# Optimization experiments

Hardware: AMD Instinct MI355X
Metric: run time of the kernel (lower is better)

The kernel has to match this reference:

```python
import jax, jax.numpy as jnp
import numpy as np

B, C, H, W = 2, 128, 48, 48
N = H * W
NQ = 25               # number of quantization bins (r2d2 default)
K_RELIABILITY = 0.5   # self.k
A = (NQ - 1) / 2.0    # quantizer slope over score range [-1, 1]
RADIUS = 4            # label window: [x-4 : x+5, y-4 : y+5]

# ---- quantizer line coefficients (r2d2 quantized AP) ----
# first half: q1 = -a*s + (a*min + [nq..1]);  special bin 0 -> constant 1
# second half: q2 =  a*s + ([2-nq..1] - a*min); special last bin -> constant 1
_W1 = jnp.full((NQ,), -A, jnp.float32).at[0].set(0.0)
_B1 = (jnp.arange(NQ, 0, -1, dtype=jnp.float32) - A).at[0].set(1.0)
_W2 = jnp.full((NQ,), A, jnp.float32).at[-1].set(0.0)
_B2 = (jnp.arange(2 - NQ, 2, dtype=jnp.float32) + A).at[-1].set(1.0)

# ---- ground-truth label matrix (static): pixel j positive for query i iff within 9x9 window ----
_row = np.arange(N) // W
_col = np.arange(N) % W
_L = ((np.abs(_row[:, None] - _row[None, :]) <= RADIUS) &
      (np.abs(_col[:, None] - _col[None, :]) <= RADIUS)).astype(np.float32)
LABEL = jnp.asarray(_L)  # (N, N)


def grid_sample_bilinear(img, grid):
    """torch.F.grid_sample: bilinear, zero padding, align_corners=False.
    img: (C, H, W); grid: (Hg, Wg, 2) in [-1, 1] -> out (C, Hg, Wg)."""
    Ci, Hi, Wi = img.shape
    ix = ((grid[..., 0] + 1.0) * Wi - 1.0) * 0.5
    iy = ((grid[..., 1] + 1.0) * Hi - 1.0) * 0.5
    x0 = jnp.floor(ix); y0 = jnp.floor(iy)
    wx1 = ix - x0; wy1 = iy - y0

    def gather(xi, yi):
        valid = (xi >= 0) & (xi < Wi) & (yi >= 0) & (yi < Hi)
        xc = jnp.clip(xi, 0, Wi - 1).astype(jnp.int32)
        yc = jnp.clip(yi, 0, Hi - 1).astype(jnp.int32)
        return img[:, yc, xc] * valid.astype(img.dtype)  # (C, Hg, Wg)

    return (gather(x0, y0) * (1 - wx1) * (1 - wy1)
            + gather(x0 + 1, y0) * wx1 * (1 - wy1)
            + gather(x0, y0 + 1) * (1 - wx1) * wy1
            + gather(x0 + 1, y0 + 1) * wx1 * wy1)


def quantized_ap(S, labels):
    """S: (N, M) similarity scores in [-1,1]; labels: (N, M) in {0,1}. Returns AP (N,)."""
    s = S[:, None, :]                                      # (N, 1, M)
    q1 = _W1[None, :, None] * s + _B1[None, :, None]        # (N, NQ, M)
    q2 = _W2[None, :, None] * s + _B2[None, :, None]
    q = jnp.maximum(jnp.minimum(q1, q2), 0.0)               # triangular bin weights
    nbs = q.sum(-1)                                         # (N, NQ) all counts per bin
    rec = jnp.einsum('ncm,nm->nc', q, labels)               # (N, NQ) positive counts per bin
    prec = jnp.cumsum(rec, -1) / (1e-16 + jnp.cumsum(nbs, -1))
    return (prec * rec).sum(-1) / rec.sum(-1)               # (N,)


def _loss_one(query_desc, db_desc, rel_map, g):
    db = grid_sample_bilinear(db_desc, g)                   # (C, H, W)
    Q = query_desc.reshape(C, N).T                          # (N, C)
    D = db.reshape(C, N).T                                  # (M=N, C)
    S = Q @ D.T                                             # (N, M) cosine scores
    ap = quantized_ap(S, LABEL)                             # (N,)
    r = rel_map.reshape(-1)                                 # (N,)
    return jnp.mean(1.0 - (ap * r + K_RELIABILITY * (1.0 - r)))


def setup_inputs() -> dict:
    key = jax.random.key(0)
    k1, k2, k3, k4 = jax.random.split(key, 4)
    d1 = jax.random.normal(k1, (B, C, H, W), jnp.float32)
    d1 = d1 / jnp.linalg.norm(d1, axis=1, keepdims=True)
    d2 = jax.random.normal(k2, (B, C, H, W), jnp.float32)
    d2 = d2 / jnp.linalg.norm(d2, axis=1, keepdims=True)
    rel = jax.random.uniform(k3, (B, 1, H, W), jnp.float32)
    grid = jax.random.uniform(k4, (B, H, W, 2), jnp.float32, minval=-1.0, maxval=1.0)
    return {"image1_descriptor": d1, "image2_descriptor": d2,
            "reliability": rel, "grid": grid}


def reference(image1_descriptor, image2_descriptor, reliability, grid):
    per_image = jax.vmap(_loss_one)(image1_descriptor, image2_descriptor,
                                    reliability[:, 0], grid)
    return per_image.mean()
```

## Files before the change

### kernel.cpp

```cpp
#include <hip/hip_runtime.h>
#include <hip/hip_bf16.h>

#define BB 2
#define CC 128
#define HH 48
#define WW 48
#define NN (HH*WW)
#define PB 26
#define HST 27
#define QT 16
#define MT 64
#define MSPLIT 4
#define NTILES (NN/QT)
#define ITERS (NN/MSPLIT/MT)
#define SLICE (QT*PB)
#define PSCALE 65536.0f
#define PINV   (1.0f/65536.0f)

typedef __bf16 bf16x8 __attribute__((ext_vector_type(8)));
typedef float  f32x4  __attribute__((ext_vector_type(4)));
typedef unsigned short u16;
typedef unsigned int   u32;

static __device__ __forceinline__ u16 f2bf(float x) {
    __hip_bfloat16 h = __float2bfloat16(x);
    return __builtin_bit_cast(u16, h);
}

__global__ __launch_bounds__(256)
void k_prep(const float* __restrict__ img1, const float* __restrict__ img2,
            const float* __restrict__ grid, u16* __restrict__ Qt,
            u16* __restrict__ Dt, float* __restrict__ out) {
    int blk = blockIdx.x;
    if (blk == 0 && threadIdx.x == 0) out[0] = 0.0f;
    bool isg = blk >= 144;
    int bb  = isg ? blk - 144 : blk;
    int bm  = (bb >> 3) * 256 + threadIdx.x;
    int cc0 = (bb & 7) * 16;
    int b   = bm / NN;
    int p   = bm - b * NN;
    u16 tmp[16];
    if (!isg) {
        const float* im = img1 + (size_t)b * CC * NN + (size_t)cc0 * NN;
        #pragma unroll
        for (int c = 0; c < 16; ++c) tmp[c] = f2bf(im[(size_t)c * NN + p]);
        uint4* dst = reinterpret_cast<uint4*>(Qt + (size_t)bm * CC + cc0);
        dst[0] = *reinterpret_cast<uint4*>(&tmp[0]);
        dst[1] = *reinterpret_cast<uint4*>(&tmp[8]);
    } else {
        float gx = grid[bm * 2 + 0];
        float gy = grid[bm * 2 + 1];
        float ix = ((gx + 1.0f) * (float)WW - 1.0f) * 0.5f;
        float iy = ((gy + 1.0f) * (float)HH - 1.0f) * 0.5f;
        float x0f = floorf(ix), y0f = floorf(iy);
        float wx1 = ix - x0f, wy1 = iy - y0f;
        float wx0 = 1.0f - wx1, wy0 = 1.0f - wy1;
        int x0 = (int)x0f, y0 = (int)y0f;
        bool xv0 = (x0 >= 0) && (x0 < WW);
        bool xv1 = (x0 + 1 >= 0) && (x0 + 1 < WW);
        bool yv0 = (y0 >= 0) && (y0 < HH);
        bool yv1 = (y0 + 1 >= 0) && (y0 + 1 < HH);
        int x0c = min(max(x0, 0), WW - 1), x1c = min(max(x0 + 1, 0), WW - 1);
        int y0c = min(max(y0, 0), HH - 1), y1c = min(max(y0 + 1, 0), HH - 1);
        float w00 = (xv0 && yv0) ? wx0 * wy0 : 0.0f;
        float w01 = (xv1 && yv0) ? wx1 * wy0 : 0.0f;
        float w10 = (xv0 && yv1) ? wx0 * wy1 : 0.0f;
        float w11 = (xv1 && yv1) ? wx1 * wy1 : 0.0f;
        int p00 = y0c * WW + x0c, p01 = y0c * WW + x1c;
        int p10 = y1c * WW + x0c, p11 = y1c * WW + x1c;
        const float* im = img2 + (size_t)b * CC * NN + (size_t)cc0 * NN;
        #pragma unroll
        for (int c = 0; c < 16; ++c) {
            const float* pl = im + (size_t)c * NN;
            tmp[c] = f2bf(pl[p00] * w00 + pl[p01] * w01 + pl[p10] * w10 + pl[p11] * w11);
        }
        uint4* dst = reinterpret_cast<uint4*>(Dt + (size_t)bm * CC + cc0);
        dst[0] = *reinterpret_cast<uint4*>(&tmp[0]);
        dst[1] = *reinterpret_cast<uint4*>(&tmp[8]);
    }
}

__global__ __launch_bounds__(256)
void k_main(const u16* __restrict__ Qt, const u16* __restrict__ Dt,
            float* __restrict__ Hall, float* __restrict__ Hpos) {
    __shared__ u16  Qs[QT * 136];
    __shared__ u16  Ds[MT * 136];
    __shared__ float priv[256 * HST];
    __shared__ u32   poshu[QT * PB];

    int tid  = threadIdx.x;
    int bidx = blockIdx.x;
    int b     = bidx / (NTILES * MSPLIT);
    int rem   = bidx % (NTILES * MSPLIT);
    int ntile = rem / MSPLIT;
    int ms    = rem % MSPLIT;
    int n0 = ntile * QT;

    for (int i = tid; i < 256 * HST; i += 256) priv[i] = 0.0f;
    for (int i = tid; i < QT * PB; i += 256) poshu[i] = 0u;
    {
        int row = tid >> 4, col = tid & 15;
        *reinterpret_cast<uint4*>(&Qs[row * 136 + col * 8]) =
            *reinterpret_cast<const uint4*>(Qt + ((size_t)(b * NN + n0 + row)) * CC + col * 8);
    }
    int lane = tid & 63, wave = tid >> 6, quad = lane >> 4, l15 = lane & 15;
    int q  = l15;
    int n  = n0 + q;
    int rn = n / WW, cn = n % WW;
    float* ph = &priv[tid * HST];

    int mstart = ms * (NN / MSPLIT);
    for (int it = 0; it < ITERS; ++it) {
        int m0 = mstart + it * MT;
        __syncthreads();
        #pragma unroll
        for (int k = 0; k < 4; ++k) {
            int idx = tid + k * 256;
            int row = idx >> 4, col = idx & 15;
            *reinterpret_cast<uint4*>(&Ds[row * 136 + col * 8]) =
                *reinterpret_cast<const uint4*>(Dt + ((size_t)(b * NN + m0 + row)) * CC + col * 8);
        }
        __syncthreads();

        f32x4 acc = {0.f, 0.f, 0.f, 0.f};
        #pragma unroll
        for (int kc = 0; kc < 4; ++kc) {
            bf16x8 av = *reinterpret_cast<const bf16x8*>(&Ds[(wave * 16 + l15) * 136 + kc * 32 + quad * 8]);
            bf16x8 bv = *reinterpret_cast<const bf16x8*>(&Qs[l15 * 136 + kc * 32 + quad * 8]);
            acc = __builtin_amdgcn_mfma_f32_16x16x32_bf16(av, bv, acc, 0, 0, 0);
        }

        int mb = m0 + wave * 16 + quad * 4;
        #pragma unroll
        for (int i = 0; i < 4; ++i) {
            float s  = acc[i];
            float t  = fminf(fmaxf(fmaf(-12.0f, s, 12.0f), 0.0f), 24.0f);
            float cf = floorf(t);
            float f  = t - cf;
            int   c0 = (int)cf;
            float h0 = ph[c0], h1 = ph[c0 + 1];
            ph[c0]     = h0 + (1.0f - f);
            ph[c0 + 1] = h1 + f;
            int m  = mb + i;
            int rm = m / WW, cm = m - rm * WW;
            int dr = rn - rm, dc = cn - cm;
            if ((unsigned)(dr + 4) <= 8u && (unsigned)(dc + 4) <= 8u) {
                u32 w0 = (u32)(fmaf(-PSCALE, f, PSCALE) + 0.5f);
                u32 w1 = (u32)(f * PSCALE + 0.5f);
                atomicAdd(&poshu[q * PB + c0],     w0);
                atomicAdd(&poshu[q * PB + c0 + 1], w1);
            }
        }
    }
    __syncthreads();
    float* oa = Hall + (size_t)bidx * SLICE;
    float* op = Hpos + (size_t)bidx * SLICE;
    for (int idx = tid; idx < SLICE; idx += 256) {
        int c = idx >> 4, qq = idx & 15;
        float s2 = 0.0f;
        #pragma unroll
        for (int j = 0; j < 16; ++j) s2 += priv[(j * 16 + qq) * HST + c];
        oa[idx] = s2;
        op[idx] = (float)poshu[qq * PB + c] * PINV;
    }
}

__global__ __launch_bounds__(256)
void k_finalize(const float* __restrict__ Hall, const float* __restrict__ Hpos,
                const float* __restrict__ rel, float* __restrict__ out) {
    int gid = blockIdx.x * 256 + threadIdx.x;
    int b = gid / NN, nloc = gid % NN;
    int ntile = nloc >> 4, qq = nloc & 15;
    size_t base = ((size_t)(b * NTILES + ntile) * MSPLIT) * SLICE + qq;
    const float* ha = Hall + base;
    const float* hp = Hpos + base;
    float cumr = 0.f, cumn = 0.f, apn = 0.f, totr = 0.f;
    #pragma unroll
    for (int c = 0; c < 25; ++c) {
        float a = 0.f, r = 0.f;
        #pragma unroll
        for (int s = 0; s < MSPLIT; ++s) {
            a += ha[(size_t)s * SLICE + c * 16];
            r += hp[(size_t)s * SLICE + c * 16];
        }
        cumr += r; cumn += a;
        apn  += (cumr / (1e-16f + cumn)) * r;
        totr += r;
    }
    float ap = apn / totr;
    float rl = rel[gid];
    float loss = 1.0f - (ap * rl + 0.5f * (1.0f - rl));

    for (int off = 32; off > 0; off >>= 1) loss += __shfl_down(loss, off, 64);
    __shared__ float wsum[4];
    int ln = threadIdx.x & 63, wv = threadIdx.x >> 6;
    if (ln == 0) wsum[wv] = loss;
    __syncthreads();
    if (threadIdx.x == 0) {
        float t = wsum[0] + wsum[1] + wsum[2] + wsum[3];
        atomicAdd(out, t * (1.0f / (float)(BB * NN)));
    }
}

extern "C" void kernel_launch(void* const* d_in, const int* in_sizes, int n_in,
                              void* d_out, int out_size, void* d_ws, size_t ws_size,
                              hipStream_t stream) {
    const float* img1 = (const float*)d_in[0];
    const float* img2 = (const float*)d_in[1];
    const float* rel  = (const float*)d_in[2];
    const float* grid = (const float*)d_in[3];

    char* ws = (char*)d_ws;
    const size_t qt_bytes   = (size_t)BB * NN * CC * sizeof(u16);
    const size_t part_bytes = (size_t)BB * NTILES * MSPLIT * SLICE * sizeof(float);
    u16*   Qt   = (u16*)ws;
    u16*   Dt   = (u16*)(ws + qt_bytes);
    float* Hall = (float*)(ws + 2 * qt_bytes);
    float* Hpos = (float*)(ws + 2 * qt_bytes + part_bytes);

    k_prep    <<<288, 256, 0, stream>>>(img1, img2, grid, Qt, Dt, (float*)d_out);
    k_main    <<<BB * NTILES * MSPLIT, 256, 0, stream>>>(Qt, Dt, Hall, Hpos);
    k_finalize<<<(BB * NN) / 256, 256, 0, stream>>>(Hall, Hpos, rel, (float*)d_out);
}
```

Before: 98.80 us.

## Load MFMA operands directly into registers and fuse finalize via last-block counter

The main kernel no longer stages Q and D tiles through shared memory. Each lane loads its bf16 operand fragments straight from global memory into registers and prefetches the next D tile one iteration ahead. This removes two barriers per iteration and the LDS tile buffers. The separate finalize kernel is replaced by an atomic per-group counter, zeroed in the prep kernel, so the last of the MSPLIT blocks for a query tile combines the partial histograms, computes AP and adds to the output. This saves a kernel launch and a pass over global memory, at the cost of thread fences, an atomic counter per group, and more redundant global loads of D rows, since they are no longer shared through LDS.

```diff
diff --git a/kernel.cpp b/kernel.cpp
--- a/kernel.cpp
+++ b/kernel.cpp
@@ -30,8 +30,9 @@
 __global__ __launch_bounds__(256)
 void k_prep(const float* __restrict__ img1, const float* __restrict__ img2,
             const float* __restrict__ grid, u16* __restrict__ Qt,
-            u16* __restrict__ Dt, float* __restrict__ out) {
+            u16* __restrict__ Dt, u32* __restrict__ cnt, float* __restrict__ out) {
     int blk = blockIdx.x;
+    if (threadIdx.x == 0) cnt[blk] = 0u;
     if (blk == 0 && threadIdx.x == 0) out[0] = 0.0f;
     bool isg = blk >= 144;
     int bb  = isg ? blk - 144 : blk;
@@ -82,11 +83,12 @@
 
 __global__ __launch_bounds__(256)
 void k_main(const u16* __restrict__ Qt, const u16* __restrict__ Dt,
-            float* __restrict__ Hall, float* __restrict__ Hpos) {
-    __shared__ u16  Qs[QT * 136];
-    __shared__ u16  Ds[MT * 136];
+            float* __restrict__ Hall, float* __restrict__ Hpos,
+            u32* __restrict__ cnt, const float* __restrict__ rel,
+            float* __restrict__ out) {
     __shared__ float priv[256 * HST];
     __shared__ u32   poshu[QT * PB];
+    __shared__ int   lastflag;
 
     int tid  = threadIdx.x;
     int bidx = blockIdx.x;
@@ -94,61 +96,67 @@
     int rem   = bidx % (NTILES * MSPLIT);
     int ntile = rem / MSPLIT;
     int ms    = rem % MSPLIT;
-    int n0 = ntile * QT;
+    int n0  = ntile * QT;
+    int grp = b * NTILES + ntile;
 
     for (int i = tid; i < 256 * HST; i += 256) priv[i] = 0.0f;
     for (int i = tid; i < QT * PB; i += 256) poshu[i] = 0u;
-    {
-        int row = tid >> 4, col = tid & 15;
-        *reinterpret_cast<uint4*>(&Qs[row * 136 + col * 8]) =
-            *reinterpret_cast<const uint4*>(Qt + ((size_t)(b * NN + n0 + row)) * CC + col * 8);
-    }
+
     int lane = tid & 63, wave = tid >> 6, quad = lane >> 4, l15 = lane & 15;
     int q  = l15;
     int n  = n0 + q;
     int rn = n / WW, cn = n % WW;
     float* ph = &priv[tid * HST];
 
+    const u16* qrow = Qt + ((size_t)(b * NN + n0 + l15)) * CC + quad * 8;
+    bf16x8 bv0 = *reinterpret_cast<const bf16x8*>(qrow);
+    bf16x8 bv1 = *reinterpret_cast<const bf16x8*>(qrow + 32);
+    bf16x8 bv2 = *reinterpret_cast<const bf16x8*>(qrow + 64);
+    bf16x8 bv3 = *reinterpret_cast<const bf16x8*>(qrow + 96);
+
+    __syncthreads();
+
     int mstart = ms * (NN / MSPLIT);
+    const u16* arow = Dt + ((size_t)(b * NN + mstart + wave * 16 + l15)) * CC + quad * 8;
+    bf16x8 a0 = *reinterpret_cast<const bf16x8*>(arow);
+    bf16x8 a1 = *reinterpret_cast<const bf16x8*>(arow + 32);
+    bf16x8 a2 = *reinterpret_cast<const bf16x8*>(arow + 64);
+    bf16x8 a3 = *reinterpret_cast<const bf16x8*>(arow + 96);
+
     for (int it = 0; it < ITERS; ++it) {
-        int m0 = mstart + it * MT;
-        __syncthreads();
-        #pragma unroll
-        for (int k = 0; k < 4; ++k) {
-            int idx = tid + k * 256;
-            int row = idx >> 4, col = idx & 15;
-            *reinterpret_cast<uint4*>(&Ds[row * 136 + col * 8]) =
-                *reinterpret_cast<const uint4*>(Dt + ((size_t)(b * NN + m0 + row)) * CC + col * 8);
-        }
-        __syncthreads();
-
+        bf16x8 c0 = a0, c1 = a1, c2 = a2, c3 = a3;
+        if (it + 1 < ITERS) {
+            const u16* nx = arow + (size_t)(it + 1) * MT * CC;
+            a0 = *reinterpret_cast<const bf16x8*>(nx);
+            a1 = *reinterpret_cast<const bf16x8*>(nx + 32);
+            a2 = *reinterpret_cast<const bf16x8*>(nx + 64);
+            a3 = *reinterpret_cast<const bf16x8*>(nx + 96);
+        }
         f32x4 acc = {0.f, 0.f, 0.f, 0.f};
-        #pragma unroll
-        for (int kc = 0; kc < 4; ++kc) {
-            bf16x8 av = *reinterpret_cast<const bf16x8*>(&Ds[(wave * 16 + l15) * 136 + kc * 32 + quad * 8]);
-            bf16x8 bv = *reinterpret_cast<const bf16x8*>(&Qs[l15 * 136 + kc * 32 + quad * 8]);
-            acc = __builtin_amdgcn_mfma_f32_16x16x32_bf16(av, bv, acc, 0, 0, 0);
-        }
-
-        int mb = m0 + wave * 16 + quad * 4;
+        acc = __builtin_amdgcn_mfma_f32_16x16x32_bf16(c0, bv0, acc, 0, 0, 0);
+        acc = __builtin_amdgcn_mfma_f32_16x16x32_bf16(c1, bv1, acc, 0, 0, 0);
+        acc = __builtin_amdgcn_mfma_f32_16x16x32_bf16(c2, bv2, acc, 0, 0, 0);
+        acc = __builtin_amdgcn_mfma_f32_16x16x32_bf16(c3, bv3, acc, 0, 0, 0);
+
+        int mb = mstart + it * MT + wave * 16 + quad * 4;
         #pragma unroll
         for (int i = 0; i < 4; ++i) {
             float s  = acc[i];
             float t  = fminf(fmaxf(fmaf(-12.0f, s, 12.0f), 0.0f), 24.0f);
             float cf = floorf(t);
             float f  = t - cf;
-            int   c0 = (int)cf;
-            float h0 = ph[c0], h1 = ph[c0 + 1];
-            ph[c0]     = h0 + (1.0f - f);
-            ph[c0 + 1] = h1 + f;
+            int   c0b = (int)cf;
+            float h0 = ph[c0b], h1 = ph[c0b + 1];
+            ph[c0b]     = h0 + (1.0f - f);
+            ph[c0b + 1] = h1 + f;
             int m  = mb + i;
             int rm = m / WW, cm = m - rm * WW;
             int dr = rn - rm, dc = cn - cm;
             if ((unsigned)(dr + 4) <= 8u && (unsigned)(dc + 4) <= 8u) {
                 u32 w0 = (u32)(fmaf(-PSCALE, f, PSCALE) + 0.5f);
                 u32 w1 = (u32)(f * PSCALE + 0.5f);
-                atomicAdd(&poshu[q * PB + c0],     w0);
-                atomicAdd(&poshu[q * PB + c0 + 1], w1);
+                atomicAdd(&poshu[q * PB + c0b],     w0);
+                atomicAdd(&poshu[q * PB + c0b + 1], w1);
             }
         }
     }
@@ -163,42 +171,46 @@
         oa[idx] = s2;
         op[idx] = (float)poshu[qq * PB + c] * PINV;
     }
-}
-
-__global__ __launch_bounds__(256)
-void k_finalize(const float* __restrict__ Hall, const float* __restrict__ Hpos,
-                const float* __restrict__ rel, float* __restrict__ out) {
-    int gid = blockIdx.x * 256 + threadIdx.x;
-    int b = gid / NN, nloc = gid % NN;
-    int ntile = nloc >> 4, qq = nloc & 15;
-    size_t base = ((size_t)(b * NTILES + ntile) * MSPLIT) * SLICE + qq;
-    const float* ha = Hall + base;
-    const float* hp = Hpos + base;
-    float cumr = 0.f, cumn = 0.f, apn = 0.f, totr = 0.f;
-    #pragma unroll
-    for (int c = 0; c < 25; ++c) {
-        float a = 0.f, r = 0.f;
+    __threadfence();
+    __syncthreads();
+    if (tid == 0) {
+        u32 old = atomicAdd(&cnt[grp], 1u);
+        lastflag = (old == MSPLIT - 1);
+    }
+    __syncthreads();
+    if (!lastflag) return;
+
+    __threadfence();
+    float* comb = priv;
+    const float* ga = Hall + (size_t)grp * MSPLIT * SLICE;
+    const float* gp = Hpos + (size_t)grp * MSPLIT * SLICE;
+    for (int idx = tid; idx < SLICE; idx += 256) {
+        float sa = 0.f, sp = 0.f;
         #pragma unroll
         for (int s = 0; s < MSPLIT; ++s) {
-            a += ha[(size_t)s * SLICE + c * 16];
-            r += hp[(size_t)s * SLICE + c * 16];
-        }
-        cumr += r; cumn += a;
-        apn  += (cumr / (1e-16f + cumn)) * r;
-        totr += r;
-    }
-    float ap = apn / totr;
-    float rl = rel[gid];
-    float loss = 1.0f - (ap * rl + 0.5f * (1.0f - rl));
-
-    for (int off = 32; off > 0; off >>= 1) loss += __shfl_down(loss, off, 64);
-    __shared__ float wsum[4];
-    int ln = threadIdx.x & 63, wv = threadIdx.x >> 6;
-    if (ln == 0) wsum[wv] = loss;
-    __syncthreads();
-    if (threadIdx.x == 0) {
-        float t = wsum[0] + wsum[1] + wsum[2] + wsum[3];
-        atomicAdd(out, t * (1.0f / (float)(BB * NN)));
+            sa += ga[(size_t)s * SLICE + idx];
+            sp += gp[(size_t)s * SLICE + idx];
+        }
+        comb[idx]         = sa;
+        comb[SLICE + idx] = sp;
+    }
+    __syncthreads();
+    if (tid < 16) {
+        float cumr = 0.f, cumn = 0.f, apn = 0.f, totr = 0.f;
+        #pragma unroll
+        for (int c = 0; c < 25; ++c) {
+            float a = comb[c * 16 + tid];
+            float r = comb[SLICE + c * 16 + tid];
+            cumr += r; cumn += a;
+            apn  += (cumr / (1e-16f + cumn)) * r;
+            totr += r;
+        }
+        float ap = apn / totr;
+        float rl = rel[b * NN + n0 + tid];
+        float loss = 1.0f - (ap * rl + 0.5f * (1.0f - rl));
+        #pragma unroll
+        for (int off = 8; off > 0; off >>= 1) loss += __shfl_down(loss, off, 16);
+        if (tid == 0) atomicAdd(out, loss * (1.0f / (float)(BB * NN)));
     }
 }
 
@@ -217,8 +229,8 @@
     u16*   Dt   = (u16*)(ws + qt_bytes);
     float* Hall = (float*)(ws + 2 * qt_bytes);
     float* Hpos = (float*)(ws + 2 * qt_bytes + part_bytes);
-
-    k_prep    <<<288, 256, 0, stream>>>(img1, img2, grid, Qt, Dt, (float*)d_out);
-    k_main    <<<BB * NTILES * MSPLIT, 256, 0, stream>>>(Qt, Dt, Hall, Hpos);
-    k_finalize<<<(BB * NN) / 256, 256, 0, stream>>>(Hall, Hpos, rel, (float*)d_out);
-}
+    u32*   cnt  = (u32*)  (ws + 2 * qt_bytes + 2 * part_bytes);
+
+    k_prep<<<288, 256, 0, stream>>>(img1, img2, grid, Qt, Dt, cnt, (float*)d_out);
+    k_main<<<BB * NTILES * MSPLIT, 256, 0, stream>>>(Qt, Dt, Hall, Hpos, cnt, rel, (float*)d_out);
+}
```

Result: slower. 225.7 us (+128.5%).

## Load MFMA operands directly from global into registers with prefetch, drop LDS staging

Applied to the files above, without the earlier changes.

Removes the shared-memory tiles for Q and D. Each wave now loads its MFMA fragments directly from global memory into registers, keeps the Q fragments resident for the whole loop, and prefetches the next D fragment while the current one is consumed. This drops two __syncthreads per iteration and the LDS round trip, and frees shared memory, which may help occupancy. The cost is per-lane 16-byte global loads with a strided row pattern and extra registers for double-buffered fragments.

```diff
diff --git a/kernel.cpp b/kernel.cpp
--- a/kernel.cpp
+++ b/kernel.cpp
@@ -83,8 +83,6 @@
 __global__ __launch_bounds__(256)
 void k_main(const u16* __restrict__ Qt, const u16* __restrict__ Dt,
             float* __restrict__ Hall, float* __restrict__ Hpos) {
-    __shared__ u16  Qs[QT * 136];
-    __shared__ u16  Ds[MT * 136];
     __shared__ float priv[256 * HST];
     __shared__ u32   poshu[QT * PB];
 
@@ -98,57 +96,62 @@
 
     for (int i = tid; i < 256 * HST; i += 256) priv[i] = 0.0f;
     for (int i = tid; i < QT * PB; i += 256) poshu[i] = 0u;
-    {
-        int row = tid >> 4, col = tid & 15;
-        *reinterpret_cast<uint4*>(&Qs[row * 136 + col * 8]) =
-            *reinterpret_cast<const uint4*>(Qt + ((size_t)(b * NN + n0 + row)) * CC + col * 8);
-    }
+
     int lane = tid & 63, wave = tid >> 6, quad = lane >> 4, l15 = lane & 15;
     int q  = l15;
     int n  = n0 + q;
     int rn = n / WW, cn = n % WW;
     float* ph = &priv[tid * HST];
 
+    const u16* qrow = Qt + ((size_t)(b * NN + n0 + l15)) * CC + quad * 8;
+    bf16x8 bv0 = *reinterpret_cast<const bf16x8*>(qrow);
+    bf16x8 bv1 = *reinterpret_cast<const bf16x8*>(qrow + 32);
+    bf16x8 bv2 = *reinterpret_cast<const bf16x8*>(qrow + 64);
+    bf16x8 bv3 = *reinterpret_cast<const bf16x8*>(qrow + 96);
+
+    __syncthreads();
+
     int mstart = ms * (NN / MSPLIT);
+    const u16* arow = Dt + ((size_t)(b * NN + mstart + wave * 16 + l15)) * CC + quad * 8;
+    bf16x8 a0 = *reinterpret_cast<const bf16x8*>(arow);
+    bf16x8 a1 = *reinterpret_cast<const bf16x8*>(arow + 32);
+    bf16x8 a2 = *reinterpret_cast<const bf16x8*>(arow + 64);
+    bf16x8 a3 = *reinterpret_cast<const bf16x8*>(arow + 96);
+
     for (int it = 0; it < ITERS; ++it) {
-        int m0 = mstart + it * MT;
-        __syncthreads();
-        #pragma unroll
-        for (int k = 0; k < 4; ++k) {
-            int idx = tid + k * 256;
-            int row = idx >> 4, col = idx & 15;
-            *reinterpret_cast<uint4*>(&Ds[row * 136 + col * 8]) =
-                *reinterpret_cast<const uint4*>(Dt + ((size_t)(b * NN + m0 + row)) * CC + col * 8);
-        }
-        __syncthreads();
-
+        bf16x8 c0v = a0, c1v = a1, c2v = a2, c3v = a3;
+        if (it + 1 < ITERS) {
+            const u16* nx = arow + (size_t)(it + 1) * MT * CC;
+            a0 = *reinterpret_cast<const bf16x8*>(nx);
+            a1 = *reinterpret_cast<const bf16x8*>(nx + 32);
+            a2 = *reinterpret_cast<const bf16x8*>(nx + 64);
+            a3 = *reinterpret_cast<const bf16x8*>(nx + 96);
+        }
         f32x4 acc = {0.f, 0.f, 0.f, 0.f};
-        #pragma unroll
-        for (int kc = 0; kc < 4; ++kc) {
-            bf16x8 av = *reinterpret_cast<const bf16x8*>(&Ds[(wave * 16 + l15) * 136 + kc * 32 + quad * 8]);
-            bf16x8 bv = *reinterpret_cast<const bf16x8*>(&Qs[l15 * 136 + kc * 32 + quad * 8]);
-            acc = __builtin_amdgcn_mfma_f32_16x16x32_bf16(av, bv, acc, 0, 0, 0);
-        }
-
-        int mb = m0 + wave * 16 + quad * 4;
+        acc = __builtin_amdgcn_mfma_f32_16x16x32_bf16(c0v, bv0, acc, 0, 0, 0);
+        acc = __builtin_amdgcn_mfma_f32_16x16x32_bf16(c1v, bv1, acc, 0, 0, 0);
+        acc = __builtin_amdgcn_mfma_f32_16x16x32_bf16(c2v, bv2, acc, 0, 0, 0);
+        acc = __builtin_amdgcn_mfma_f32_16x16x32_bf16(c3v, bv3, acc, 0, 0, 0);
+
+        int mb = mstart + it * MT + wave * 16 + quad * 4;
         #pragma unroll
         for (int i = 0; i < 4; ++i) {
             float s  = acc[i];
             float t  = fminf(fmaxf(fmaf(-12.0f, s, 12.0f), 0.0f), 24.0f);
             float cf = floorf(t);
             float f  = t - cf;
-            int   c0 = (int)cf;
-            float h0 = ph[c0], h1 = ph[c0 + 1];
-            ph[c0]     = h0 + (1.0f - f);
-            ph[c0 + 1] = h1 + f;
+            int   c0b = (int)cf;
+            float h0 = ph[c0b], h1 = ph[c0b + 1];
+            ph[c0b]     = h0 + (1.0f - f);
+            ph[c0b + 1] = h1 + f;
             int m  = mb + i;
             int rm = m / WW, cm = m - rm * WW;
             int dr = rn - rm, dc = cn - cm;
             if ((unsigned)(dr + 4) <= 8u && (unsigned)(dc + 4) <= 8u) {
                 u32 w0 = (u32)(fmaf(-PSCALE, f, PSCALE) + 0.5f);
                 u32 w1 = (u32)(f * PSCALE + 0.5f);
-                atomicAdd(&poshu[q * PB + c0],     w0);
-                atomicAdd(&poshu[q * PB + c0 + 1], w1);
+                atomicAdd(&poshu[q * PB + c0b],     w0);
+                atomicAdd(&poshu[q * PB + c0b + 1], w1);
             }
         }
     }
```

Measured after the change: 99.76 us. Within noise of the previous version (+1.0%).
